# Performance work log

Hardware: AMD Instinct MI355X
Metric: run time of the kernel (lower is better)

Reference implementation:

```python
import jax, jax.numpy as jnp
import numpy as np

OUT = 7
N, C, HMAX, WMAX = 512, 256, 14, 14


def setup_inputs() -> dict:
    key = jax.random.key(0)
    k1, k2, k3 = jax.random.split(key, 3)
    rois = jax.random.normal(k1, (N, C, HMAX, WMAX), dtype=jnp.float32)
    # valid ROI sizes in [7, 14] (padded up to HMAX/WMAX)
    h = jax.random.randint(k2, (N,), 7, HMAX + 1, dtype=jnp.int32)
    w = jax.random.randint(k3, (N,), 7, WMAX + 1, dtype=jnp.int32)
    return {"rois": rois, "h": h, "w": w}


def _bin_mask(sizes, max_len):
    # sizes: [N] valid lengths. Returns [N, OUT, max_len] bool membership mask
    # matching nn.AdaptiveMaxPool2d: bin i covers [floor(i*L/OUT), ceil((i+1)*L/OUT))
    i = jnp.arange(OUT, dtype=jnp.int32)[None, :]          # [1, OUT]
    L = sizes[:, None]                                      # [N, 1]
    start = (i * L) // OUT                                  # [N, OUT]
    end = ((i + 1) * L + OUT - 1) // OUT                    # ceil, [N, OUT]
    r = jnp.arange(max_len, dtype=jnp.int32)[None, None, :]  # [1, 1, max_len]
    return (r >= start[:, :, None]) & (r < end[:, :, None])  # [N, OUT, max_len]


def reference(rois, h, w):
    neg = jnp.finfo(rois.dtype).min
    mh = _bin_mask(h, HMAX)  # [N, OUT, HMAX]
    mw = _bin_mask(w, WMAX)  # [N, OUT, WMAX]
    # max over rows per row-bin: [N, C, OUT, WMAX]
    rowp = jnp.max(jnp.where(mh[:, None, :, :, None], rois[:, :, None, :, :], neg), axis=3)
    # max over cols per col-bin: [N, C, OUT, OUT]
    out = jnp.max(jnp.where(mw[:, None, None, :, :], rowp[:, :, :, None, :], neg), axis=4)
    # original: torch.cat of per-ROI [C, OUT, OUT] along dim 0 -> [N*C, OUT, OUT]
    return out.reshape(N * C, OUT, OUT)
```

## Files before the change

kernel.cpp:

```cpp
#include <hip/hip_runtime.h>
#include <float.h>


constexpr int N_   = 512;
constexpr int C_   = 256;
constexpr int WMAX = 14;
constexpr int OUT  = 7;
constexpr int PLANE = 196;
constexpr int P     = 16;
constexpr int NBLK  = (N_ * C_) / P;
constexpr int NOUT  = P * OUT * OUT;

template<int LW>
__device__ __forceinline__ void hpool(const float (&vm)[WMAX], float (&o)[OUT]) {
    #pragma unroll
    for (int j = 0; j < OUT; ++j) {
        int c1 = (j * LW) / 7;
        int c3 = ((j + 1) * LW + 6) / 7 - 1;
        int c2 = (c1 + 1 < c3) ? c1 + 1 : c3;
        o[j] = fmaxf(fmaxf(vm[c1], vm[c2]), vm[c3]);
    }
}

__global__ __launch_bounds__(256) void roipool_kernel(
    const float* __restrict__ rois,
    const int*   __restrict__ h,
    const int*   __restrict__ w,
    float*       __restrict__ out)
{
    __shared__ float lds[P * PLANE];
    __shared__ float ostage[NOUT];

    const int tid = threadIdx.x;
    const int blk = blockIdx.x;

    const int n  = blk >> 4;
    const int Lh = h[n];
    const int Lw = w[n];
    const int V  = (7 * Lh + 1) >> 1;

    {
        const float4* src = (const float4*)rois + (size_t)blk * (NOUT);
        float4* ldsv = (float4*)lds;
        int p = tid >> 4;
        int l = tid & 15;
        int base = p * 49;
        for (int v = l; v < V; v += 16)
            ldsv[base + v] = src[base + v];
    }
    __syncthreads();

    if (tid < P * OUT) {
        int p = tid / 7;
        int i = tid - p * 7;

        int th = i * Lh;
        int r1 = th / 7;
        int r3 = (th + Lh + 6) / 7 - 1;
        int r2 = min(r1 + 1, r3);

        const float2* a = (const float2*)(lds + p * PLANE + r1 * WMAX);
        const float2* b = (const float2*)(lds + p * PLANE + r2 * WMAX);
        const float2* c = (const float2*)(lds + p * PLANE + r3 * WMAX);

        float vm[WMAX];
        #pragma unroll
        for (int k = 0; k < 7; ++k) {
            float2 x = a[k], y = b[k], z = c[k];
            vm[2 * k]     = fmaxf(fmaxf(x.x, y.x), z.x);
            vm[2 * k + 1] = fmaxf(fmaxf(x.y, y.y), z.y);
        }

        float o[OUT];
        switch (Lw) {
            case  7: hpool< 7>(vm, o); break;
            case  8: hpool< 8>(vm, o); break;
            case  9: hpool< 9>(vm, o); break;
            case 10: hpool<10>(vm, o); break;
            case 11: hpool<11>(vm, o); break;
            case 12: hpool<12>(vm, o); break;
            case 13: hpool<13>(vm, o); break;
            default: hpool<14>(vm, o); break;
        }

        float* os = ostage + tid * OUT;
        #pragma unroll
        for (int j = 0; j < OUT; ++j) os[j] = o[j];
    }
    __syncthreads();

    if (tid < NOUT / 4) {
        float4 v = ((const float4*)ostage)[tid];
        ((float4*)out)[(size_t)blk * (NOUT / 4) + tid] = v;
    }
}

extern "C" void kernel_launch(void* const* d_in, const int* in_sizes, int n_in,
                              void* d_out, int out_size, void* d_ws, size_t ws_size,
                              hipStream_t stream)
{
    const float* rois = (const float*)d_in[0];
    const int*   h    = (const int*)d_in[1];
    const int*   w    = (const int*)d_in[2];
    float*       out  = (float*)d_out;

    roipool_kernel<<<NBLK, 256, 0, stream>>>(rois, h, w, out);
}
```

Baseline: 25.14 us.

## Make ROI pool kernel persistent with double-buffered async global-to-LDS loads

The grid shrinks to 1024 blocks, and each block loops over 8 tiles of 16 planes. The next tile is prefetched into a second LDS buffer with global_load_lds direct-to-LDS copies. Explicit vmcnt waits and barriers ensure the current tile has landed before compute, while the next tile's loads and the previous tile's stores stay in flight. The aim is to overlap global memory latency with pooling and to cut per-block launch and sync overhead. In exchange it relies on hand-counted vmcnt values, raises LDS use per block, and gives fewer blocks in total to hide latency.

```diff
diff --git a/kernel.cpp b/kernel.cpp
--- a/kernel.cpp
+++ b/kernel.cpp
@@ -1,15 +1,20 @@
 #include <hip/hip_runtime.h>
-#include <float.h>
 
 
-constexpr int N_   = 512;
-constexpr int C_   = 256;
-constexpr int WMAX = 14;
-constexpr int OUT  = 7;
-constexpr int PLANE = 196;
+constexpr int N_    = 512;
+constexpr int C_    = 256;
+constexpr int WMAX  = 14;
+constexpr int OUT   = 7;
 constexpr int P     = 16;
-constexpr int NBLK  = (N_ * C_) / P;
+constexpr int NTILE = (N_ * C_) / P;
+constexpr int G     = 1024;
+constexpr int T     = NTILE / G;
+constexpr int PS4   = 65;
+constexpr int PSF   = PS4 * 4;
 constexpr int NOUT  = P * OUT * OUT;
+
+typedef const __attribute__((address_space(1))) unsigned int* gas_u32;
+typedef __attribute__((address_space(3))) unsigned int* las_u32;
 
 template<int LW>
 __device__ __forceinline__ void hpool(const float (&vm)[WMAX], float (&o)[OUT]) {
@@ -28,70 +33,98 @@
     const int*   __restrict__ w,
     float*       __restrict__ out)
 {
-    __shared__ float lds[P * PLANE];
-    __shared__ float ostage[NOUT];
+    __shared__ float4 buf[2][P * PS4];
+    __shared__ float  ostage[NOUT];
 
-    const int tid = threadIdx.x;
-    const int blk = blockIdx.x;
+    const int tid  = threadIdx.x;
+    const int lane = tid & 63;
+    const int wv   = tid >> 6;
+    const int blk  = blockIdx.x;
 
-    const int n  = blk >> 4;
-    const int Lh = h[n];
-    const int Lw = w[n];
-    const int V  = (7 * Lh + 1) >> 1;
+    int LH[T], LWv[T];
+    #pragma unroll
+    for (int k = 0; k < T; ++k) {
+        int n = (blk >> 4) + 64 * k;
+        LH[k]  = h[n];
+        LWv[k] = w[n];
+    }
 
-    {
-        const float4* src = (const float4*)rois + (size_t)blk * (NOUT);
-        float4* ldsv = (float4*)lds;
-        int p = tid >> 4;
-        int l = tid & 15;
-        int base = p * 49;
-        for (int v = l; v < V; v += 16)
-            ldsv[base + v] = src[base + v];
-    }
-    __syncthreads();
+    auto stage = [&](int k, int b) {
+        const float4* src = (const float4*)rois + (size_t)(blk + k * G) * (P * 49);
+        const int V = (7 * LH[k] + 1) >> 1;
+        #pragma unroll
+        for (int s = 0; s < 4; ++s) {
+            const int p  = 4 * wv + s;
+            const int l2 = (lane < V) ? lane : 0;
+            if (lane < V) {
+                __builtin_amdgcn_global_load_lds(
+                    (gas_u32)(src + p * 49 + l2),
+                    (las_u32)(&buf[b][p * PS4]),
+                    16, 0, 0);
+            }
+        }
+    };
 
-    if (tid < P * OUT) {
-        int p = tid / 7;
-        int i = tid - p * 7;
+    stage(0, 0);
 
-        int th = i * Lh;
-        int r1 = th / 7;
-        int r3 = (th + Lh + 6) / 7 - 1;
-        int r2 = min(r1 + 1, r3);
+    #pragma unroll
+    for (int t = 0; t < T; ++t) {
+        if (t + 1 < T) stage(t + 1, (t + 1) & 1);
 
-        const float2* a = (const float2*)(lds + p * PLANE + r1 * WMAX);
-        const float2* b = (const float2*)(lds + p * PLANE + r2 * WMAX);
-        const float2* c = (const float2*)(lds + p * PLANE + r3 * WMAX);
+        if (t == 0)          asm volatile("s_waitcnt vmcnt(4)" ::: "memory");
+        else if (t == T - 1) asm volatile("s_waitcnt vmcnt(1)" ::: "memory");
+        else                 asm volatile("s_waitcnt vmcnt(5)" ::: "memory");
+        __builtin_amdgcn_s_barrier();
+        asm volatile("" ::: "memory");
 
-        float vm[WMAX];
-        #pragma unroll
-        for (int k = 0; k < 7; ++k) {
-            float2 x = a[k], y = b[k], z = c[k];
-            vm[2 * k]     = fmaxf(fmaxf(x.x, y.x), z.x);
-            vm[2 * k + 1] = fmaxf(fmaxf(x.y, y.y), z.y);
+        if (tid < P * OUT) {
+            const int p  = tid / 7;
+            const int i  = tid - p * 7;
+            const int Lh = LH[t];
+
+            int th = i * Lh;
+            int r1 = th / 7;
+            int r3 = (th + Lh + 6) / 7 - 1;
+            int r2 = min(r1 + 1, r3);
+
+            const float*  pb = (const float*)&buf[t & 1][0] + p * PSF;
+            const float2* a  = (const float2*)(pb + r1 * WMAX);
+            const float2* bb = (const float2*)(pb + r2 * WMAX);
+            const float2* c  = (const float2*)(pb + r3 * WMAX);
+
+            float vm[WMAX];
+            #pragma unroll
+            for (int kk = 0; kk < 7; ++kk) {
+                float2 x = a[kk], y = bb[kk], z = c[kk];
+                vm[2 * kk]     = fmaxf(fmaxf(x.x, y.x), z.x);
+                vm[2 * kk + 1] = fmaxf(fmaxf(x.y, y.y), z.y);
+            }
+
+            float o[OUT];
+            switch (LWv[t]) {
+                case  7: hpool< 7>(vm, o); break;
+                case  8: hpool< 8>(vm, o); break;
+                case  9: hpool< 9>(vm, o); break;
+                case 10: hpool<10>(vm, o); break;
+                case 11: hpool<11>(vm, o); break;
+                case 12: hpool<12>(vm, o); break;
+                case 13: hpool<13>(vm, o); break;
+                default: hpool<14>(vm, o); break;
+            }
+
+            float* os = ostage + tid * OUT;
+            #pragma unroll
+            for (int j = 0; j < OUT; ++j) os[j] = o[j];
         }
 
-        float o[OUT];
-        switch (Lw) {
-            case  7: hpool< 7>(vm, o); break;
-            case  8: hpool< 8>(vm, o); break;
-            case  9: hpool< 9>(vm, o); break;
-            case 10: hpool<10>(vm, o); break;
-            case 11: hpool<11>(vm, o); break;
-            case 12: hpool<12>(vm, o); break;
-            case 13: hpool<13>(vm, o); break;
-            default: hpool<14>(vm, o); break;
+        asm volatile("s_waitcnt lgkmcnt(0)" ::: "memory");
+        __builtin_amdgcn_s_barrier();
+        asm volatile("" ::: "memory");
+
+        if (tid < NOUT / 4) {
+            ((float4*)out)[(size_t)(blk + t * G) * (NOUT / 4) + tid] =
+                ((const float4*)ostage)[tid];
         }
-
-        float* os = ostage + tid * OUT;
-        #pragma unroll
-        for (int j = 0; j < OUT; ++j) os[j] = o[j];
-    }
-    __syncthreads();
-
-    if (tid < NOUT / 4) {
-        float4 v = ((const float4*)ostage)[tid];
-        ((float4*)out)[(size_t)blk * (NOUT / 4) + tid] = v;
     }
 }
 
@@ -104,5 +137,5 @@
     const int*   w    = (const int*)d_in[2];
     float*       out  = (float*)d_out;
 
-    roipool_kernel<<<NBLK, 256, 0, stream>>>(rois, h, w, out);
+    roipool_kernel<<<G, 256, 0, stream>>>(rois, h, w, out);
 }
```

Measured after the change: 24.46 us. 2.7% less time.
